# Kernel tuning notes

Hardware: AMD Instinct MI355X
Metric: run time of the kernel (lower is better)

The kernel has to match this reference:

```python
import jax, jax.numpy as jnp
import numpy as np

N_NODES = 50000
N_EDGES = 800000
F_IN = 512
HID = 256
N_CLS = 40
W_DIM = 50  # dimension*dimension*2 with dimension=5


def _prelu(x, a):
    return jnp.where(x >= 0, x, a * x)


def _segment_softmax(w, idx, n):
    # per-segment (grouped by idx), per-channel numerically stable softmax
    m = jax.ops.segment_max(w, idx, num_segments=n)
    e = jnp.exp(w - m[idx])
    s = jax.ops.segment_sum(e, idx, num_segments=n)
    return e / s[idx]


def _curvgn(x, edge_index, w_mul, W, b, w0, a, w1, b1):
    n = x.shape[0]
    h = x @ W + b                                   # [N, C]
    ow = _prelu(w_mul @ w0, a) @ w1 + b1            # [E, C] edge-weight MLP
    ow = _segment_softmax(ow, edge_index[0], n)     # softmax grouped by source (as in source)
    msg = ow * h[edge_index[0]]                     # gather x_j, weight
    return jax.ops.segment_sum(msg, edge_index[1], num_segments=n)  # scatter-add at target


def setup_inputs() -> dict:
    key = jax.random.key(0)
    ks = jax.random.split(key, 12)
    s = 0.05
    return {
        "x": jax.random.normal(ks[0], (N_NODES, F_IN), jnp.float32),
        "edge_index": jax.random.randint(ks[1], (2, N_EDGES), 0, N_NODES, jnp.int64 if jax.config.jax_enable_x64 else jnp.int32).astype(jnp.int32),
        "w_mul": jax.random.normal(ks[2], (N_EDGES, W_DIM), jnp.float32),
        "W1": jax.random.normal(ks[3], (F_IN, HID), jnp.float32) * s,
        "b1": jnp.zeros((HID,), jnp.float32),
        "m1_w0": jax.random.normal(ks[4], (W_DIM, HID), jnp.float32) * s,
        "m1_a": jnp.full((HID,), 0.2, jnp.float32),
        "m1_w1": jax.random.normal(ks[5], (HID, HID), jnp.float32) * s,
        "m1_b1": jnp.zeros((HID,), jnp.float32),
        "W2": jax.random.normal(ks[6], (HID, N_CLS), jnp.float32) * s,
        "b2": jnp.zeros((N_CLS,), jnp.float32),
        "m2_w0": jax.random.normal(ks[7], (W_DIM, N_CLS), jnp.float32) * s,
        "m2_a": jnp.full((N_CLS,), 0.2, jnp.float32),
        "m2_w1": jax.random.normal(ks[8], (N_CLS, N_CLS), jnp.float32) * s,
        "m2_b1": jnp.zeros((N_CLS,), jnp.float32),
    }


def reference(x, edge_index, w_mul, W1, b1, m1_w0, m1_a, m1_w1, m1_b1,
              W2, b2, m2_w0, m2_a, m2_w1, m2_b1):
    # eval mode: dropout is identity
    h = _curvgn(x, edge_index, w_mul, W1, b1, m1_w0, m1_a, m1_w1, m1_b1)
    h = jax.nn.elu(h)
    out = _curvgn(h, edge_index, w_mul, W2, b2, m2_w0, m2_a, m2_w1, m2_b1)
    return jax.nn.log_softmax(out, axis=1)
```

## Files before the change

### kernel.cpp

```cpp
#include <hip/hip_runtime.h>
#include <hip/hip_bf16.h>
#include <math.h>

#define N_NODESC 50000
#define N_EDGESC 800000
#define F_INC 512
#define HIDC 256
#define N_CLSC 40
#define W_DIMC 50
#define HN (2*N_NODESC)
#define NB_SCAN 196

typedef __bf16 bf16;
typedef __bf16 bf16x8 __attribute__((ext_vector_type(8)));
typedef __bf16 bf16x4 __attribute__((ext_vector_type(4)));
typedef float  f32x4  __attribute__((ext_vector_type(4)));

__global__ void k_hist(const int* __restrict__ ei, int* __restrict__ hist) {
    int e = blockIdx.x*256 + threadIdx.x;
    if (e < N_EDGESC) {
        atomicAdd(&hist[ei[e]], 1);
        atomicAdd(&hist[N_NODESC + ei[N_EDGESC + e]], 1);
    }
}
__global__ void k_copy(int* d, const int* s, int n) {
    int i = blockIdx.x*256 + threadIdx.x;
    if (i < n) d[i] = s[i];
}
__global__ void k_scan_part(const int* __restrict__ hist, int* __restrict__ part) {
    __shared__ int lds[512];
    int t = threadIdx.x;
    int i = blockIdx.x*512 + t;
    lds[t] = (i < HN) ? hist[i] : 0;
    __syncthreads();
    for (int off = 256; off > 0; off >>= 1) {
        if (t < off) lds[t] += lds[t+off];
        __syncthreads();
    }
    if (t == 0) part[blockIdx.x] = lds[0];
}
__global__ void k_scan_mid(const int* __restrict__ part, int* __restrict__ partx) {
    __shared__ int lds[256];
    int t = threadIdx.x;
    int v = (t < NB_SCAN) ? part[t] : 0;
    lds[t] = v;
    __syncthreads();
    for (int off = 1; off < 256; off <<= 1) {
        int add = (t >= off) ? lds[t-off] : 0;
        __syncthreads();
        lds[t] += add;
        __syncthreads();
    }
    partx[t] = lds[t] - v;
}
__global__ void k_scan_apply(const int* __restrict__ hist, const int* __restrict__ partx,
                             int* __restrict__ basev) {
    __shared__ int lds[512];
    int t = threadIdx.x;
    int i = blockIdx.x*512 + t;
    int v = (i < HN) ? hist[i] : 0;
    lds[t] = v;
    __syncthreads();
    for (int off = 1; off < 512; off <<= 1) {
        int add = (t >= off) ? lds[t-off] : 0;
        __syncthreads();
        lds[t] += add;
        __syncthreads();
    }
    if (i < HN) basev[i] = lds[t] - v + partx[blockIdx.x];
}
__global__ void k_scatter(const int* __restrict__ ei, int* __restrict__ cursor,
                          int* __restrict__ perm_src, int* __restrict__ perm_dst,
                          int* __restrict__ pos_dst) {
    int e = blockIdx.x*256 + threadIdx.x;
    if (e >= N_EDGESC) return;
    int s = ei[e];
    int d = ei[N_EDGESC + e];
    int p = atomicAdd(&cursor[s], 1);
    perm_src[p] = e;
    int q = atomicAdd(&cursor[N_NODESC + d], 1) - N_EDGESC;
    perm_dst[q] = e;
    pos_dst[e] = q;
}

__global__ void k_tconv(const float* __restrict__ src, bf16* __restrict__ dst,
                        int Ks, int Ns, int Kp, int Np) {
    int idx = blockIdx.x*256 + threadIdx.x;
    if (idx >= Kp*Np) return;
    int n = idx / Kp, k = idx - n*Kp;
    float v = (k < Ks && n < Ns) ? src[k*Ns + n] : 0.f;
    dst[idx] = (bf16)v;
}

__global__ __launch_bounds__(256) void k_h1(const float* __restrict__ x,
                                            const bf16* __restrict__ W1t,
                                            const float* __restrict__ b1,
                                            bf16* __restrict__ h1) {
    __shared__ bf16 a_lds[64*40];
    int tid = threadIdx.x;
    int lane = tid & 63, wv = tid >> 6;
    int l15 = lane & 15, quad = lane >> 4;
    int r0 = blockIdx.x * 64;
    f32x4 acc[4][4] = {};
    for (int ks = 0; ks < 16; ++ks) {
        #pragma unroll
        for (int i = 0; i < 2; ++i) {
            int idx = tid + i*256;
            int rl = idx >> 3, c4 = idx & 7;
            int rg = r0 + rl;
            f32x4 v = {};
            if (rg < N_NODESC) v = *(const f32x4*)&x[rg*F_INC + ks*32 + c4*4];
            bf16x4 b; b[0]=(bf16)v[0]; b[1]=(bf16)v[1]; b[2]=(bf16)v[2]; b[3]=(bf16)v[3];
            *(bf16x4*)&a_lds[rl*40 + c4*4] = b;
        }
        __syncthreads();
        bf16x8 af[4], bfr[4];
        #pragma unroll
        for (int mt = 0; mt < 4; ++mt)
            af[mt] = *(const bf16x8*)&a_lds[(mt*16 + l15)*40 + quad*8];
        #pragma unroll
        for (int nt = 0; nt < 4; ++nt) {
            int n = wv*64 + nt*16 + l15;
            bfr[nt] = *(const bf16x8*)&W1t[n*F_INC + ks*32 + quad*8];
        }
        #pragma unroll
        for (int mt = 0; mt < 4; ++mt)
            #pragma unroll
            for (int nt = 0; nt < 4; ++nt)
                acc[mt][nt] = __builtin_amdgcn_mfma_f32_16x16x32_bf16(af[mt], bfr[nt], acc[mt][nt], 0, 0, 0);
        __syncthreads();
    }
    #pragma unroll
    for (int nt = 0; nt < 4; ++nt) {
        int col = wv*64 + nt*16 + l15;
        float bias = b1[col];
        #pragma unroll
        for (int mt = 0; mt < 4; ++mt)
            #pragma unroll
            for (int r = 0; r < 4; ++r) {
                int row = r0 + mt*16 + quad*4 + r;
                if (row < N_NODESC) h1[row*HIDC + col] = (bf16)(acc[mt][nt][r] + bias);
            }
    }
}

__device__ __forceinline__ void edge_mlp1(
    int tid, const bf16* __restrict__ w0t, const float* __restrict__ a1,
    const bf16* __restrict__ w1t, const float* __restrict__ bb1,
    const bf16* wm, bf16* t1)
{
    int lane = tid & 63, wv = tid >> 6;
    int l15 = lane & 15, quad = lane >> 4;
    {
        f32x4 acc[4][4] = {};
        #pragma unroll
        for (int ks = 0; ks < 2; ++ks) {
            bf16x8 af[4], bfr[4];
            #pragma unroll
            for (int mt = 0; mt < 4; ++mt)
                af[mt] = *(const bf16x8*)&wm[(mt*16 + l15)*72 + ks*32 + quad*8];
            #pragma unroll
            for (int i = 0; i < 4; ++i) {
                int n = wv*64 + i*16 + l15;
                bfr[i] = *(const bf16x8*)&w0t[n*64 + ks*32 + quad*8];
            }
            #pragma unroll
            for (int mt = 0; mt < 4; ++mt)
                #pragma unroll
                for (int i = 0; i < 4; ++i)
                    acc[mt][i] = __builtin_amdgcn_mfma_f32_16x16x32_bf16(af[mt], bfr[i], acc[mt][i], 0, 0, 0);
        }
        #pragma unroll
        for (int i = 0; i < 4; ++i) {
            int col = wv*64 + i*16 + l15;
            float al = a1[col];
            #pragma unroll
            for (int mt = 0; mt < 4; ++mt)
                #pragma unroll
                for (int r = 0; r < 4; ++r) {
                    float v = acc[mt][i][r];
                    v = (v >= 0.f) ? v : al*v;
                    t1[(mt*16 + quad*4 + r)*264 + col] = (bf16)v;
                }
        }
    }
    __syncthreads();
    {
        f32x4 acc[4][4] = {};
        #pragma unroll
        for (int ks = 0; ks < 8; ++ks) {
            bf16x8 af[4], bfr[4];
            #pragma unroll
            for (int mt = 0; mt < 4; ++mt)
                af[mt] = *(const bf16x8*)&t1[(mt*16 + l15)*264 + ks*32 + quad*8];
            #pragma unroll
            for (int i = 0; i < 4; ++i) {
                int n = wv*64 + i*16 + l15;
                bfr[i] = *(const bf16x8*)&w1t[n*HIDC + ks*32 + quad*8];
            }
            #pragma unroll
            for (int mt = 0; mt < 4; ++mt)
                #pragma unroll
                for (int i = 0; i < 4; ++i)
                    acc[mt][i] = __builtin_amdgcn_mfma_f32_16x16x32_bf16(af[mt], bfr[i], acc[mt][i], 0, 0, 0);
        }
        __syncthreads();
        #pragma unroll
        for (int i = 0; i < 4; ++i) {
            int col = wv*64 + i*16 + l15;
            float bias = bb1[col];
            #pragma unroll
            for (int mt = 0; mt < 4; ++mt)
                #pragma unroll
                for (int r = 0; r < 4; ++r)
                    t1[(mt*16 + quad*4 + r)*264 + col] = (bf16)__expf(acc[mt][i][r] + bias);
        }
    }
    __syncthreads();
}

__device__ __forceinline__ void edge_mlp2(
    int tid, const bf16* __restrict__ w20t, const float* __restrict__ a2,
    const bf16* __restrict__ w21t, const float* __restrict__ bb2,
    const bf16* wm, bf16* t2)
{
    int lane = tid & 63, wv = tid >> 6;
    int l15 = lane & 15, quad = lane >> 4;
    {
        f32x4 acc[3] = {};
        #pragma unroll
        for (int ks = 0; ks < 2; ++ks) {
            bf16x8 af = *(const bf16x8*)&wm[(wv*16 + l15)*72 + ks*32 + quad*8];
            #pragma unroll
            for (int i = 0; i < 3; ++i) {
                bf16x8 bfr = *(const bf16x8*)&w20t[(i*16 + l15)*64 + ks*32 + quad*8];
                acc[i] = __builtin_amdgcn_mfma_f32_16x16x32_bf16(af, bfr, acc[i], 0, 0, 0);
            }
        }
        #pragma unroll
        for (int i = 0; i < 3; ++i) {
            int col = i*16 + l15;
            float al = (col < N_CLSC) ? a2[col] : 0.f;
            #pragma unroll
            for (int r = 0; r < 4; ++r) {
                float v = acc[i][r];
                v = (v >= 0.f) ? v : al*v;
                t2[(wv*16 + quad*4 + r)*72 + col] = (bf16)v;
            }
        }
    }
    __syncthreads();
    {
        f32x4 acc[3] = {};
        #pragma unroll
        for (int ks = 0; ks < 2; ++ks) {
            bf16x8 af = *(const bf16x8*)&t2[(wv*16 + l15)*72 + ks*32 + quad*8];
            #pragma unroll
            for (int i = 0; i < 3; ++i) {
                bf16x8 bfr = *(const bf16x8*)&w21t[(i*16 + l15)*64 + ks*32 + quad*8];
                acc[i] = __builtin_amdgcn_mfma_f32_16x16x32_bf16(af, bfr, acc[i], 0, 0, 0);
            }
        }
        __syncthreads();
        #pragma unroll
        for (int i = 0; i < 3; ++i) {
            int col = i*16 + l15;
            if (col < N_CLSC) {
                float bias = bb2[col];
                #pragma unroll
                for (int r = 0; r < 4; ++r)
                    t2[(wv*16 + quad*4 + r)*72 + col] = (bf16)__expf(acc[i][r] + bias);
            }
        }
    }
    __syncthreads();
}

__global__ __launch_bounds__(256) void k_passA(
    const float* __restrict__ w_mul, const int* __restrict__ perm_src,
    const int* __restrict__ ei, const int* __restrict__ pos_dst,
    const bf16* __restrict__ w0t,  const float* __restrict__ a1,
    const bf16* __restrict__ w1t,  const float* __restrict__ bb1,
    const bf16* __restrict__ w20t, const float* __restrict__ a2,
    const bf16* __restrict__ w21t, const float* __restrict__ bb2,
    float* __restrict__ s1, float* __restrict__ s2,
    bf16* __restrict__ eow1buf, bf16* __restrict__ eow2buf) {
    __shared__ bf16 wm[64*72];
    __shared__ bf16 t1[64*264];
    __shared__ bf16 t2[64*72];
    __shared__ int  e_lds[64], sv[64], pd[64];
    int tid = threadIdx.x;
    int p0 = blockIdx.x * 64;

    if (tid < 64) {
        int e = perm_src[p0 + tid];
        e_lds[tid] = e;
        sv[tid] = ei[e];
        pd[tid] = pos_dst[e];
    }
    __syncthreads();
    #pragma unroll
    for (int i = 0; i < 16; ++i) {
        int idx = tid + i*256;
        int r = idx >> 6, k = idx & 63;
        float v = (k < W_DIMC) ? w_mul[(size_t)e_lds[r]*W_DIMC + k] : 0.f;
        wm[r*72 + k] = (bf16)v;
    }
    #pragma unroll
    for (int i = 0; i < 4; ++i) {
        int idx = tid + i*256;
        int r = idx >> 4, c = 48 + (idx & 15);
        t2[r*72 + c] = (bf16)0.f;
    }
    __syncthreads();

    edge_mlp1(tid, w0t, a1, w1t, bb1, wm, t1);

    if (eow1buf) {
        int c = tid;
        for (int r = 0; r < 64; ++r)
            eow1buf[(size_t)pd[r]*HIDC + c] = t1[r*264 + c];
    }
    {
        int c = tid, r = 0;
        while (r < 64) {
            int v = sv[r];
            float acc = 0.f;
            do { acc += (float)t1[r*264 + c]; ++r; } while (r < 64 && sv[r] == v);
            atomicAdd(&s1[(size_t)v*HIDC + c], acc);
        }
    }
    __syncthreads();

    edge_mlp2(tid, w20t, a2, w21t, bb2, wm, t2);

    if (eow2buf && tid < N_CLSC) {
        int c = tid;
        for (int r = 0; r < 64; ++r)
            eow2buf[(size_t)pd[r]*N_CLSC + c] = t2[r*72 + c];
    }
    if (tid < N_CLSC) {
        int c = tid, r = 0;
        while (r < 64) {
            int v = sv[r];
            float acc = 0.f;
            do { acc += (float)t2[r*72 + c]; ++r; } while (r < 64 && sv[r] == v);
            atomicAdd(&s2[(size_t)v*N_CLSC + c], acc);
        }
    }
}

__global__ __launch_bounds__(256) void k_passB1(
    const float* __restrict__ w_mul, const int* __restrict__ perm_dst,
    const int* __restrict__ ei,
    const bf16* __restrict__ w0t, const float* __restrict__ a1,
    const bf16* __restrict__ w1t, const float* __restrict__ bb1,
    const bf16* __restrict__ g1, float* __restrict__ out1) {
    __shared__ bf16 wm[64*72];
    __shared__ bf16 t1[64*264];
    __shared__ int  e_lds[64], sv[64], dv[64];
    int tid = threadIdx.x;
    int q0 = blockIdx.x * 64;

    if (tid < 64) {
        int e = perm_dst[q0 + tid];
        e_lds[tid] = e;
        sv[tid] = ei[e];
        dv[tid] = ei[N_EDGESC + e];
    }
    __syncthreads();
    #pragma unroll
    for (int i = 0; i < 16; ++i) {
        int idx = tid + i*256;
        int r = idx >> 6, k = idx & 63;
        float v = (k < W_DIMC) ? w_mul[(size_t)e_lds[r]*W_DIMC + k] : 0.f;
        wm[r*72 + k] = (bf16)v;
    }
    __syncthreads();

    edge_mlp1(tid, w0t, a1, w1t, bb1, wm, t1);

    int c = tid, r = 0;
    while (r < 64) {
        int d = dv[r];
        float acc = 0.f;
        do {
            acc += (float)t1[r*264 + c] * (float)g1[(size_t)sv[r]*HIDC + c];
            ++r;
        } while (r < 64 && dv[r] == d);
        atomicAdd(&out1[(size_t)d*HIDC + c], acc);
    }
}
__global__ __launch_bounds__(256) void k_passB1c(
    const int* __restrict__ perm_dst, const int* __restrict__ ei,
    const bf16* __restrict__ eow1buf,
    const bf16* __restrict__ g1, float* __restrict__ out1) {
    __shared__ int sv[64], dv[64];
    int tid = threadIdx.x;
    int q0 = blockIdx.x * 64;
    if (tid < 64) {
        int e = perm_dst[q0 + tid];
        sv[tid] = ei[e];
        dv[tid] = ei[N_EDGESC + e];
    }
    __syncthreads();
    int c = tid, r = 0;
    while (r < 64) {
        int d = dv[r];
        float acc = 0.f;
        do {
            acc += (float)eow1buf[(size_t)(q0 + r)*HIDC + c] * (float)g1[(size_t)sv[r]*HIDC + c];
            ++r;
        } while (r < 64 && dv[r] == d);
        atomicAdd(&out1[(size_t)d*HIDC + c], acc);
    }
}

__global__ __launch_bounds__(256) void k_passB2(
    const float* __restrict__ w_mul, const int* __restrict__ perm_dst,
    const int* __restrict__ ei,
    const bf16* __restrict__ w20t, const float* __restrict__ a2,
    const bf16* __restrict__ w21t, const float* __restrict__ bb2,
    const bf16* __restrict__ g2, float* __restrict__ out2) {
    __shared__ bf16 wm[64*72];
    __shared__ bf16 t2[64*72];
    __shared__ int  e_lds[64], sv[64], dv[64];
    int tid = threadIdx.x;
    int q0 = blockIdx.x * 64;

    if (tid < 64) {
        int e = perm_dst[q0 + tid];
        e_lds[tid] = e;
        sv[tid] = ei[e];
        dv[tid] = ei[N_EDGESC + e];
    }
    __syncthreads();
    #pragma unroll
    for (int i = 0; i < 16; ++i) {
        int idx = tid + i*256;
        int r = idx >> 6, k = idx & 63;
        float v = (k < W_DIMC) ? w_mul[(size_t)e_lds[r]*W_DIMC + k] : 0.f;
        wm[r*72 + k] = (bf16)v;
    }
    #pragma unroll
    for (int i = 0; i < 4; ++i) {
        int idx = tid + i*256;
        int r = idx >> 4, c = 48 + (idx & 15);
        t2[r*72 + c] = (bf16)0.f;
    }
    __syncthreads();

    edge_mlp2(tid, w20t, a2, w21t, bb2, wm, t2);

    if (tid < N_CLSC) {
        int c = tid, r = 0;
        while (r < 64) {
            int d = dv[r];
            float acc = 0.f;
            do {
                acc += (float)t2[r*72 + c] * (float)g2[(size_t)sv[r]*N_CLSC + c];
                ++r;
            } while (r < 64 && dv[r] == d);
            atomicAdd(&out2[(size_t)d*N_CLSC + c], acc);
        }
    }
}
__global__ void k_passB2c(
    const int* __restrict__ perm_dst, const int* __restrict__ ei,
    const bf16* __restrict__ eow2buf,
    const bf16* __restrict__ g2, float* __restrict__ out2) {
    __shared__ int sv[64], dv[64];
    int tid = threadIdx.x;
    int q0 = blockIdx.x * 64;
    {
        int e = perm_dst[q0 + tid];
        sv[tid] = ei[e];
        dv[tid] = ei[N_EDGESC + e];
    }
    __syncthreads();
    if (tid >= N_CLSC) return;
    int c = tid, r = 0;
    while (r < 64) {
        int d = dv[r];
        float acc = 0.f;
        do {
            acc += (float)eow2buf[(size_t)(q0 + r)*N_CLSC + c] * (float)g2[(size_t)sv[r]*N_CLSC + c];
            ++r;
        } while (r < 64 && dv[r] == d);
        atomicAdd(&out2[(size_t)d*N_CLSC + c], acc);
    }
}

__global__ void k_div_bf(bf16* __restrict__ h, const float* __restrict__ s, int n) {
    int i = blockIdx.x*256 + threadIdx.x;
    if (i < n) h[i] = (bf16)((float)h[i] / s[i]);
}
__global__ void k_elu(float* __restrict__ p, int n) {
    int i = blockIdx.x*256 + threadIdx.x;
    if (i < n) { float x = p[i]; p[i] = (x > 0.f) ? x : expm1f(x); }
}
__global__ void k_h2(const float* __restrict__ out1, const float* __restrict__ W2,
                     const float* __restrict__ b2, bf16* __restrict__ h2) {
    int i = blockIdx.x*256 + threadIdx.x;
    if (i >= N_NODESC*N_CLSC) return;
    int v = i / N_CLSC, c = i - v*N_CLSC;
    float acc = b2[c];
    const float* row = &out1[(size_t)v*HIDC];
    #pragma unroll 4
    for (int k = 0; k < HIDC; ++k) acc += row[k] * W2[k*N_CLSC + c];
    h2[i] = (bf16)acc;
}
__global__ void k_lsm(const float* __restrict__ out2, float* __restrict__ out) {
    int v = blockIdx.x, c = threadIdx.x;
    bool act = (c < N_CLSC);
    float val = act ? out2[(size_t)v*N_CLSC + c] : -INFINITY;
    float m = val;
    #pragma unroll
    for (int off = 32; off > 0; off >>= 1) m = fmaxf(m, __shfl_xor(m, off));
    float ex = act ? __expf(val - m) : 0.f;
    #pragma unroll
    for (int off = 32; off > 0; off >>= 1) ex += __shfl_xor(ex, off);
    if (act) out[(size_t)v*N_CLSC + c] = val - m - logf(ex);
}

extern "C" void kernel_launch(void* const* d_in, const int* in_sizes, int n_in,
                              void* d_out, int out_size, void* d_ws, size_t ws_size,
                              hipStream_t stream) {
    const float* x    = (const float*)d_in[0];
    const int*   ei   = (const int*)d_in[1];
    const float* wmul = (const float*)d_in[2];
    const float* W1   = (const float*)d_in[3];
    const float* b1   = (const float*)d_in[4];
    const float* m1w0 = (const float*)d_in[5];
    const float* m1a  = (const float*)d_in[6];
    const float* m1w1 = (const float*)d_in[7];
    const float* m1b1 = (const float*)d_in[8];
    const float* W2   = (const float*)d_in[9];
    const float* b2   = (const float*)d_in[10];
    const float* m2w0 = (const float*)d_in[11];
    const float* m2a  = (const float*)d_in[12];
    const float* m2w1 = (const float*)d_in[13];
    const float* m2b1 = (const float*)d_in[14];
    float* out = (float*)d_out;

    char* ws = (char*)d_ws;
    size_t off = 0;
    auto alloc = [&](size_t bytes) -> void* {
        off = (off + 255) & ~(size_t)255;
        void* p = ws + off;
        off += bytes;
        return p;
    };
    bf16*  h1g1  = (bf16*) alloc((size_t)N_NODESC*HIDC*2);
    float* s1o1  = (float*)alloc((size_t)N_NODESC*HIDC*4);
    bf16*  h2g2  = (bf16*) alloc((size_t)N_NODESC*N_CLSC*2);
    float* s2o2  = (float*)alloc((size_t)N_NODESC*N_CLSC*4);
    bf16*  W1t   = (bf16*) alloc(256*512*2);
    bf16*  w0t   = (bf16*) alloc(256*64*2);
    bf16*  w1tm  = (bf16*) alloc(256*256*2);
    bf16*  w20t  = (bf16*) alloc(48*64*2);
    bf16*  w21t  = (bf16*) alloc(48*64*2);
    int*   hist  = (int*)  alloc(HN*4);
    int*   basev = (int*)  alloc(HN*4);
    int*   cursor= (int*)  alloc(HN*4);
    int*   part  = (int*)  alloc(256*4);
    int*   partx = (int*)  alloc(256*4);
    int*   perm_src = (int*)alloc((size_t)N_EDGESC*4);
    int*   perm_dst = (int*)alloc((size_t)N_EDGESC*4);
    int*   pos_dst  = (int*)alloc((size_t)N_EDGESC*4);
    size_t need_cache = (size_t)N_EDGESC*HIDC*2 + (size_t)N_EDGESC*N_CLSC*2 + 512;
    bool use_cache = (off + need_cache) <= ws_size;
    bf16* eow1buf = nullptr;
    bf16* eow2buf = nullptr;
    if (use_cache) {
        eow1buf = (bf16*)alloc((size_t)N_EDGESC*HIDC*2);
        eow2buf = (bf16*)alloc((size_t)N_EDGESC*N_CLSC*2);
    }

    hipMemsetAsync(hist, 0, HN*4, stream);
    hipMemsetAsync(s1o1, 0, (size_t)N_NODESC*HIDC*4, stream);
    hipMemsetAsync(s2o2, 0, (size_t)N_NODESC*N_CLSC*4, stream);
    k_hist<<<(N_EDGESC+255)/256, 256, 0, stream>>>(ei, hist);
    k_scan_part<<<NB_SCAN, 512, 0, stream>>>(hist, part);
    k_scan_mid<<<1, 256, 0, stream>>>(part, partx);
    k_scan_apply<<<NB_SCAN, 512, 0, stream>>>(hist, partx, basev);
    k_copy<<<(HN+255)/256, 256, 0, stream>>>(cursor, basev, HN);
    k_scatter<<<(N_EDGESC+255)/256, 256, 0, stream>>>(ei, cursor, perm_src, perm_dst, pos_dst);

    k_tconv<<<(512*256+255)/256, 256, 0, stream>>>(W1,   W1t, 512, 256, 512, 256);
    k_tconv<<<(256*64+255)/256,  256, 0, stream>>>(m1w0, w0t,  50, 256,  64, 256);
    k_tconv<<<(256*256+255)/256, 256, 0, stream>>>(m1w1, w1tm, 256, 256, 256, 256);
    k_tconv<<<(48*64+255)/256,   256, 0, stream>>>(m2w0, w20t,  50,  40,  64,  48);
    k_tconv<<<(48*64+255)/256,   256, 0, stream>>>(m2w1, w21t,  40,  40,  64,  48);

    k_h1<<<(N_NODESC+63)/64, 256, 0, stream>>>(x, W1t, b1, h1g1);
    k_passA<<<N_EDGESC/64, 256, 0, stream>>>(wmul, perm_src, ei, pos_dst,
                                             w0t, m1a, w1tm, m1b1,
                                             w20t, m2a, w21t, m2b1,
                                             s1o1, s2o2, eow1buf, eow2buf);
    k_div_bf<<<(N_NODESC*HIDC+255)/256, 256, 0, stream>>>(h1g1, s1o1, N_NODESC*HIDC);
    hipMemsetAsync(s1o1, 0, (size_t)N_NODESC*HIDC*4, stream);
    if (use_cache)
        k_passB1c<<<N_EDGESC/64, 256, 0, stream>>>(perm_dst, ei, eow1buf, h1g1, s1o1);
    else
        k_passB1<<<N_EDGESC/64, 256, 0, stream>>>(wmul, perm_dst, ei,
                                                  w0t, m1a, w1tm, m1b1, h1g1, s1o1);
    k_elu<<<(N_NODESC*HIDC+255)/256, 256, 0, stream>>>(s1o1, N_NODESC*HIDC);

    k_h2<<<(N_NODESC*N_CLSC+255)/256, 256, 0, stream>>>(s1o1, W2, b2, h2g2);
    k_div_bf<<<(N_NODESC*N_CLSC+255)/256, 256, 0, stream>>>(h2g2, s2o2, N_NODESC*N_CLSC);
    hipMemsetAsync(s2o2, 0, (size_t)N_NODESC*N_CLSC*4, stream);
    if (use_cache)
        k_passB2c<<<N_EDGESC/64, 64, 0, stream>>>(perm_dst, ei, eow2buf, h2g2, s2o2);
    else
        k_passB2<<<N_EDGESC/64, 256, 0, stream>>>(wmul, perm_dst, ei,
                                                  w20t, m2a, w21t, m2b1, h2g2, s2o2);
    k_lsm<<<N_NODESC, 64, 0, stream>>>(s2o2, out);
}
```

Measured before the change: 1.816 ms.

## Store edge weights in source order and aggregate per destination via CSR gather

The edge-MLP kernel now writes the exponentiated edge weights contiguously in source-sorted order instead of scattering them to destination positions. The scatter step records, for each destination-sorted slot, the source-sorted position and the source node. New per-node gather kernels (one block per destination node) then sum weight times feature with no atomics, and they also absorb the ELU and log-softmax epilogues. This removes the output memsets, the atomic scatter-add, the separate elementwise kernels and the non-cached fallback path, and it vectorises the divide kernel. In exchange the gathers read the weight rows indirectly, per-node blocks are unbalanced by degree, and the weight cache is now allocated unconditionally, which assumes the workspace is large enough.

```diff
diff --git a/kernel.cpp b/kernel.cpp
--- a/kernel.cpp
+++ b/kernel.cpp
@@ -70,8 +70,8 @@
     if (i < HN) basev[i] = lds[t] - v + partx[blockIdx.x];
 }
 __global__ void k_scatter(const int* __restrict__ ei, int* __restrict__ cursor,
-                          int* __restrict__ perm_src, int* __restrict__ perm_dst,
-                          int* __restrict__ pos_dst) {
+                          int* __restrict__ perm_src,
+                          int* __restrict__ spd, int* __restrict__ svd) {
     int e = blockIdx.x*256 + threadIdx.x;
     if (e >= N_EDGESC) return;
     int s = ei[e];
@@ -79,8 +79,8 @@
     int p = atomicAdd(&cursor[s], 1);
     perm_src[p] = e;
     int q = atomicAdd(&cursor[N_NODESC + d], 1) - N_EDGESC;
-    perm_dst[q] = e;
-    pos_dst[e] = q;
+    spd[q] = p;
+    svd[q] = s;
 }
 
 __global__ void k_tconv(const float* __restrict__ src, bf16* __restrict__ dst,
@@ -96,7 +96,7 @@
                                             const bf16* __restrict__ W1t,
                                             const float* __restrict__ b1,
                                             bf16* __restrict__ h1) {
-    __shared__ bf16 a_lds[64*40];
+    __shared__ __align__(16) bf16 a_lds[64*40];
     int tid = threadIdx.x;
     int lane = tid & 63, wv = tid >> 6;
     int l15 = lane & 15, quad = lane >> 4;
@@ -109,7 +109,7 @@
             int rl = idx >> 3, c4 = idx & 7;
             int rg = r0 + rl;
             f32x4 v = {};
-            if (rg < N_NODESC) v = *(const f32x4*)&x[rg*F_INC + ks*32 + c4*4];
+            if (rg < N_NODESC) v = *(const f32x4*)&x[(size_t)rg*F_INC + ks*32 + c4*4];
             bf16x4 b; b[0]=(bf16)v[0]; b[1]=(bf16)v[1]; b[2]=(bf16)v[2]; b[3]=(bf16)v[3];
             *(bf16x4*)&a_lds[rl*40 + c4*4] = b;
         }
@@ -139,18 +139,50 @@
             #pragma unroll
             for (int r = 0; r < 4; ++r) {
                 int row = r0 + mt*16 + quad*4 + r;
-                if (row < N_NODESC) h1[row*HIDC + col] = (bf16)(acc[mt][nt][r] + bias);
-            }
-    }
-}
-
-__device__ __forceinline__ void edge_mlp1(
-    int tid, const bf16* __restrict__ w0t, const float* __restrict__ a1,
-    const bf16* __restrict__ w1t, const float* __restrict__ bb1,
-    const bf16* wm, bf16* t1)
-{
+                if (row < N_NODESC) h1[(size_t)row*HIDC + col] = (bf16)(acc[mt][nt][r] + bias);
+            }
+    }
+}
+
+__global__ __launch_bounds__(256) void k_edge(
+    const float* __restrict__ w_mul, const int* __restrict__ perm_src,
+    const int* __restrict__ ei,
+    const bf16* __restrict__ w0t,  const float* __restrict__ a1,
+    const bf16* __restrict__ w1t,  const float* __restrict__ bb1,
+    const bf16* __restrict__ w20t, const float* __restrict__ a2,
+    const bf16* __restrict__ w21t, const float* __restrict__ bb2,
+    float* __restrict__ s1, float* __restrict__ s2,
+    bf16* __restrict__ eow1, bf16* __restrict__ eow2) {
+    __shared__ __align__(16) bf16 wm[64*72];
+    __shared__ __align__(16) bf16 t1[64*264];
+    __shared__ __align__(16) bf16 t2[64*72];
+    __shared__ int e_lds[64], sv[64];
+    int tid = threadIdx.x;
     int lane = tid & 63, wv = tid >> 6;
     int l15 = lane & 15, quad = lane >> 4;
+    int p0 = blockIdx.x * 64;
+
+    if (tid < 64) {
+        int e = perm_src[p0 + tid];
+        e_lds[tid] = e;
+        sv[tid] = ei[e];
+    }
+    __syncthreads();
+    #pragma unroll
+    for (int i = 0; i < 16; ++i) {
+        int idx = tid + i*256;
+        int r = idx >> 6, k = idx & 63;
+        float v = (k < W_DIMC) ? w_mul[(size_t)e_lds[r]*W_DIMC + k] : 0.f;
+        wm[r*72 + k] = (bf16)v;
+    }
+    #pragma unroll
+    for (int i = 0; i < 4; ++i) {
+        int idx = tid + i*256;
+        int r = idx >> 4, c = 48 + (idx & 15);
+        t2[r*72 + c] = (bf16)0.f;
+    }
+    __syncthreads();
+
     {
         f32x4 acc[4][4] = {};
         #pragma unroll
@@ -185,6 +217,7 @@
         }
     }
     __syncthreads();
+
     {
         f32x4 acc[4][4] = {};
         #pragma unroll
@@ -217,15 +250,27 @@
         }
     }
     __syncthreads();
-}
-
-__device__ __forceinline__ void edge_mlp2(
-    int tid, const bf16* __restrict__ w20t, const float* __restrict__ a2,
-    const bf16* __restrict__ w21t, const float* __restrict__ bb2,
-    const bf16* wm, bf16* t2)
-{
-    int lane = tid & 63, wv = tid >> 6;
-    int l15 = lane & 15, quad = lane >> 4;
+
+    #pragma unroll
+    for (int i = 0; i < 8; ++i) {
+        int idx = i*256 + tid;
+        int row = idx >> 5, c8 = idx & 31;
+        bf16x8 v = *(const bf16x8*)&t1[row*264 + c8*8];
+        *(bf16x8*)&eow1[(size_t)(p0 + row)*HIDC + c8*8] = v;
+    }
+    {
+        int c = tid;
+        float acc = 0.f;
+        #pragma unroll 8
+        for (int r = 0; r < 64; ++r) {
+            acc += (float)t1[r*264 + c];
+            if (r == 63 || sv[r+1] != sv[r]) {
+                atomicAdd(&s1[(size_t)sv[r]*HIDC + c], acc);
+                acc = 0.f;
+            }
+        }
+    }
+
     {
         f32x4 acc[3] = {};
         #pragma unroll
@@ -250,6 +295,7 @@
         }
     }
     __syncthreads();
+
     {
         f32x4 acc[3] = {};
         #pragma unroll
@@ -274,230 +320,78 @@
         }
     }
     __syncthreads();
-}
-
-__global__ __launch_bounds__(256) void k_passA(
-    const float* __restrict__ w_mul, const int* __restrict__ perm_src,
-    const int* __restrict__ ei, const int* __restrict__ pos_dst,
-    const bf16* __restrict__ w0t,  const float* __restrict__ a1,
-    const bf16* __restrict__ w1t,  const float* __restrict__ bb1,
-    const bf16* __restrict__ w20t, const float* __restrict__ a2,
-    const bf16* __restrict__ w21t, const float* __restrict__ bb2,
-    float* __restrict__ s1, float* __restrict__ s2,
-    bf16* __restrict__ eow1buf, bf16* __restrict__ eow2buf) {
-    __shared__ bf16 wm[64*72];
-    __shared__ bf16 t1[64*264];
-    __shared__ bf16 t2[64*72];
-    __shared__ int  e_lds[64], sv[64], pd[64];
-    int tid = threadIdx.x;
-    int p0 = blockIdx.x * 64;
-
-    if (tid < 64) {
-        int e = perm_src[p0 + tid];
-        e_lds[tid] = e;
-        sv[tid] = ei[e];
-        pd[tid] = pos_dst[e];
-    }
-    __syncthreads();
-    #pragma unroll
-    for (int i = 0; i < 16; ++i) {
-        int idx = tid + i*256;
-        int r = idx >> 6, k = idx & 63;
-        float v = (k < W_DIMC) ? w_mul[(size_t)e_lds[r]*W_DIMC + k] : 0.f;
-        wm[r*72 + k] = (bf16)v;
-    }
-    #pragma unroll
-    for (int i = 0; i < 4; ++i) {
-        int idx = tid + i*256;
-        int r = idx >> 4, c = 48 + (idx & 15);
-        t2[r*72 + c] = (bf16)0.f;
-    }
-    __syncthreads();
-
-    edge_mlp1(tid, w0t, a1, w1t, bb1, wm, t1);
-
-    if (eow1buf) {
-        int c = tid;
-        for (int r = 0; r < 64; ++r)
-            eow1buf[(size_t)pd[r]*HIDC + c] = t1[r*264 + c];
-    }
-    {
-        int c = tid, r = 0;
-        while (r < 64) {
-            int v = sv[r];
-            float acc = 0.f;
-            do { acc += (float)t1[r*264 + c]; ++r; } while (r < 64 && sv[r] == v);
-            atomicAdd(&s1[(size_t)v*HIDC + c], acc);
-        }
-    }
-    __syncthreads();
-
-    edge_mlp2(tid, w20t, a2, w21t, bb2, wm, t2);
-
-    if (eow2buf && tid < N_CLSC) {
-        int c = tid;
-        for (int r = 0; r < 64; ++r)
-            eow2buf[(size_t)pd[r]*N_CLSC + c] = t2[r*72 + c];
-    }
-    if (tid < N_CLSC) {
-        int c = tid, r = 0;
-        while (r < 64) {
-            int v = sv[r];
-            float acc = 0.f;
-            do { acc += (float)t2[r*72 + c]; ++r; } while (r < 64 && sv[r] == v);
-            atomicAdd(&s2[(size_t)v*N_CLSC + c], acc);
-        }
-    }
-}
-
-__global__ __launch_bounds__(256) void k_passB1(
-    const float* __restrict__ w_mul, const int* __restrict__ perm_dst,
-    const int* __restrict__ ei,
-    const bf16* __restrict__ w0t, const float* __restrict__ a1,
-    const bf16* __restrict__ w1t, const float* __restrict__ bb1,
-    const bf16* __restrict__ g1, float* __restrict__ out1) {
-    __shared__ bf16 wm[64*72];
-    __shared__ bf16 t1[64*264];
-    __shared__ int  e_lds[64], sv[64], dv[64];
-    int tid = threadIdx.x;
-    int q0 = blockIdx.x * 64;
-
-    if (tid < 64) {
-        int e = perm_dst[q0 + tid];
-        e_lds[tid] = e;
-        sv[tid] = ei[e];
-        dv[tid] = ei[N_EDGESC + e];
-    }
-    __syncthreads();
-    #pragma unroll
-    for (int i = 0; i < 16; ++i) {
-        int idx = tid + i*256;
-        int r = idx >> 6, k = idx & 63;
-        float v = (k < W_DIMC) ? w_mul[(size_t)e_lds[r]*W_DIMC + k] : 0.f;
-        wm[r*72 + k] = (bf16)v;
-    }
-    __syncthreads();
-
-    edge_mlp1(tid, w0t, a1, w1t, bb1, wm, t1);
-
-    int c = tid, r = 0;
-    while (r < 64) {
-        int d = dv[r];
+
+    #pragma unroll
+    for (int i = 0; i < 2; ++i) {
+        int idx = i*256 + tid;
+        if (idx < 320) {
+            int row = idx / 5, c8 = idx % 5;
+            bf16x8 v = *(const bf16x8*)&t2[row*72 + c8*8];
+            *(bf16x8*)&eow2[(size_t)(p0 + row)*N_CLSC + c8*8] = v;
+        }
+    }
+    if (tid < 240) {
+        int c = tid % 40, g = tid / 40;
+        int rA = g*11, rB = (rA + 11 < 64) ? rA + 11 : 64;
         float acc = 0.f;
-        do {
-            acc += (float)t1[r*264 + c] * (float)g1[(size_t)sv[r]*HIDC + c];
-            ++r;
-        } while (r < 64 && dv[r] == d);
-        atomicAdd(&out1[(size_t)d*HIDC + c], acc);
-    }
-}
-__global__ __launch_bounds__(256) void k_passB1c(
-    const int* __restrict__ perm_dst, const int* __restrict__ ei,
-    const bf16* __restrict__ eow1buf,
-    const bf16* __restrict__ g1, float* __restrict__ out1) {
-    __shared__ int sv[64], dv[64];
-    int tid = threadIdx.x;
-    int q0 = blockIdx.x * 64;
-    if (tid < 64) {
-        int e = perm_dst[q0 + tid];
-        sv[tid] = ei[e];
-        dv[tid] = ei[N_EDGESC + e];
-    }
-    __syncthreads();
-    int c = tid, r = 0;
-    while (r < 64) {
-        int d = dv[r];
-        float acc = 0.f;
-        do {
-            acc += (float)eow1buf[(size_t)(q0 + r)*HIDC + c] * (float)g1[(size_t)sv[r]*HIDC + c];
-            ++r;
-        } while (r < 64 && dv[r] == d);
-        atomicAdd(&out1[(size_t)d*HIDC + c], acc);
-    }
-}
-
-__global__ __launch_bounds__(256) void k_passB2(
-    const float* __restrict__ w_mul, const int* __restrict__ perm_dst,
-    const int* __restrict__ ei,
-    const bf16* __restrict__ w20t, const float* __restrict__ a2,
-    const bf16* __restrict__ w21t, const float* __restrict__ bb2,
-    const bf16* __restrict__ g2, float* __restrict__ out2) {
-    __shared__ bf16 wm[64*72];
-    __shared__ bf16 t2[64*72];
-    __shared__ int  e_lds[64], sv[64], dv[64];
-    int tid = threadIdx.x;
-    int q0 = blockIdx.x * 64;
-
-    if (tid < 64) {
-        int e = perm_dst[q0 + tid];
-        e_lds[tid] = e;
-        sv[tid] = ei[e];
-        dv[tid] = ei[N_EDGESC + e];
-    }
-    __syncthreads();
-    #pragma unroll
-    for (int i = 0; i < 16; ++i) {
-        int idx = tid + i*256;
-        int r = idx >> 6, k = idx & 63;
-        float v = (k < W_DIMC) ? w_mul[(size_t)e_lds[r]*W_DIMC + k] : 0.f;
-        wm[r*72 + k] = (bf16)v;
-    }
-    #pragma unroll
-    for (int i = 0; i < 4; ++i) {
-        int idx = tid + i*256;
-        int r = idx >> 4, c = 48 + (idx & 15);
-        t2[r*72 + c] = (bf16)0.f;
-    }
-    __syncthreads();
-
-    edge_mlp2(tid, w20t, a2, w21t, bb2, wm, t2);
-
-    if (tid < N_CLSC) {
-        int c = tid, r = 0;
-        while (r < 64) {
-            int d = dv[r];
-            float acc = 0.f;
-            do {
-                acc += (float)t2[r*72 + c] * (float)g2[(size_t)sv[r]*N_CLSC + c];
-                ++r;
-            } while (r < 64 && dv[r] == d);
-            atomicAdd(&out2[(size_t)d*N_CLSC + c], acc);
-        }
-    }
-}
-__global__ void k_passB2c(
-    const int* __restrict__ perm_dst, const int* __restrict__ ei,
-    const bf16* __restrict__ eow2buf,
-    const bf16* __restrict__ g2, float* __restrict__ out2) {
-    __shared__ int sv[64], dv[64];
-    int tid = threadIdx.x;
-    int q0 = blockIdx.x * 64;
-    {
-        int e = perm_dst[q0 + tid];
-        sv[tid] = ei[e];
-        dv[tid] = ei[N_EDGESC + e];
-    }
-    __syncthreads();
-    if (tid >= N_CLSC) return;
-    int c = tid, r = 0;
-    while (r < 64) {
-        int d = dv[r];
-        float acc = 0.f;
-        do {
-            acc += (float)eow2buf[(size_t)(q0 + r)*N_CLSC + c] * (float)g2[(size_t)sv[r]*N_CLSC + c];
-            ++r;
-        } while (r < 64 && dv[r] == d);
-        atomicAdd(&out2[(size_t)d*N_CLSC + c], acc);
-    }
-}
-
-__global__ void k_div_bf(bf16* __restrict__ h, const float* __restrict__ s, int n) {
+        for (int r = rA; r < rB; ++r) {
+            acc += (float)t2[r*72 + c];
+            if (r == rB-1 || sv[r+1] != sv[r]) {
+                atomicAdd(&s2[(size_t)sv[r]*N_CLSC + c], acc);
+                acc = 0.f;
+            }
+        }
+    }
+}
+
+__global__ __launch_bounds__(256) void k_agg1(
+    const bf16* __restrict__ eow1, const bf16* __restrict__ g1,
+    const int* __restrict__ basev, const int* __restrict__ spd,
+    const int* __restrict__ svd, float* __restrict__ out1) {
+    int v = blockIdx.x, c = threadIdx.x;
+    int b = basev[N_NODESC + v] - N_EDGESC;
+    int e = (v < N_NODESC-1) ? basev[N_NODESC + v + 1] - N_EDGESC : N_EDGESC;
+    float acc = 0.f;
+    #pragma unroll 2
+    for (int j = b; j < e; ++j) {
+        int sp = spd[j], s = svd[j];
+        acc += (float)eow1[(size_t)sp*HIDC + c] * (float)g1[(size_t)s*HIDC + c];
+    }
+    out1[(size_t)v*HIDC + c] = (acc > 0.f) ? acc : expm1f(acc);
+}
+
+__global__ __launch_bounds__(64) void k_agg2(
+    const bf16* __restrict__ eow2, const bf16* __restrict__ g2,
+    const int* __restrict__ basev, const int* __restrict__ spd,
+    const int* __restrict__ svd, float* __restrict__ out) {
+    int v = blockIdx.x, c = threadIdx.x;
+    int b = basev[N_NODESC + v] - N_EDGESC;
+    int e = (v < N_NODESC-1) ? basev[N_NODESC + v + 1] - N_EDGESC : N_EDGESC;
+    bool act = (c < N_CLSC);
+    float acc = 0.f;
+    #pragma unroll 2
+    for (int j = b; j < e; ++j) {
+        int sp = spd[j], s = svd[j];
+        if (act) acc += (float)eow2[(size_t)sp*N_CLSC + c] * (float)g2[(size_t)s*N_CLSC + c];
+    }
+    float m = act ? acc : -INFINITY;
+    #pragma unroll
+    for (int off = 32; off > 0; off >>= 1) m = fmaxf(m, __shfl_xor(m, off));
+    float ex = act ? __expf(acc - m) : 0.f;
+    #pragma unroll
+    for (int off = 32; off > 0; off >>= 1) ex += __shfl_xor(ex, off);
+    if (act) out[(size_t)v*N_CLSC + c] = acc - m - logf(ex);
+}
+
+__global__ void k_div_bf4(bf16* __restrict__ h, const float* __restrict__ s, int n4) {
     int i = blockIdx.x*256 + threadIdx.x;
-    if (i < n) h[i] = (bf16)((float)h[i] / s[i]);
-}
-__global__ void k_elu(float* __restrict__ p, int n) {
-    int i = blockIdx.x*256 + threadIdx.x;
-    if (i < n) { float x = p[i]; p[i] = (x > 0.f) ? x : expm1f(x); }
+    if (i < n4) {
+        bf16x4 hv = *(bf16x4*)&h[i*4];
+        f32x4 sv = *(const f32x4*)&s[i*4];
+        #pragma unroll
+        for (int k = 0; k < 4; ++k) hv[k] = (bf16)((float)hv[k] / sv[k]);
+        *(bf16x4*)&h[i*4] = hv;
+    }
 }
 __global__ void k_h2(const float* __restrict__ out1, const float* __restrict__ W2,
                      const float* __restrict__ b2, bf16* __restrict__ h2) {
@@ -509,18 +403,6 @@
     #pragma unroll 4
     for (int k = 0; k < HIDC; ++k) acc += row[k] * W2[k*N_CLSC + c];
     h2[i] = (bf16)acc;
-}
-__global__ void k_lsm(const float* __restrict__ out2, float* __restrict__ out) {
-    int v = blockIdx.x, c = threadIdx.x;
-    bool act = (c < N_CLSC);
-    float val = act ? out2[(size_t)v*N_CLSC + c] : -INFINITY;
-    float m = val;
-    #pragma unroll
-    for (int off = 32; off > 0; off >>= 1) m = fmaxf(m, __shfl_xor(m, off));
-    float ex = act ? __expf(val - m) : 0.f;
-    #pragma unroll
-    for (int off = 32; off > 0; off >>= 1) ex += __shfl_xor(ex, off);
-    if (act) out[(size_t)v*N_CLSC + c] = val - m - logf(ex);
 }
 
 extern "C" void kernel_launch(void* const* d_in, const int* in_sizes, int n_in,
@@ -554,7 +436,7 @@
     bf16*  h1g1  = (bf16*) alloc((size_t)N_NODESC*HIDC*2);
     float* s1o1  = (float*)alloc((size_t)N_NODESC*HIDC*4);
     bf16*  h2g2  = (bf16*) alloc((size_t)N_NODESC*N_CLSC*2);
-    float* s2o2  = (float*)alloc((size_t)N_NODESC*N_CLSC*4);
+    float* s2    = (float*)alloc((size_t)N_NODESC*N_CLSC*4);
     bf16*  W1t   = (bf16*) alloc(256*512*2);
     bf16*  w0t   = (bf16*) alloc(256*64*2);
     bf16*  w1tm  = (bf16*) alloc(256*256*2);
@@ -566,26 +448,20 @@
     int*   part  = (int*)  alloc(256*4);
     int*   partx = (int*)  alloc(256*4);
     int*   perm_src = (int*)alloc((size_t)N_EDGESC*4);
-    int*   perm_dst = (int*)alloc((size_t)N_EDGESC*4);
-    int*   pos_dst  = (int*)alloc((size_t)N_EDGESC*4);
-    size_t need_cache = (size_t)N_EDGESC*HIDC*2 + (size_t)N_EDGESC*N_CLSC*2 + 512;
-    bool use_cache = (off + need_cache) <= ws_size;
-    bf16* eow1buf = nullptr;
-    bf16* eow2buf = nullptr;
-    if (use_cache) {
-        eow1buf = (bf16*)alloc((size_t)N_EDGESC*HIDC*2);
-        eow2buf = (bf16*)alloc((size_t)N_EDGESC*N_CLSC*2);
-    }
+    int*   spd      = (int*)alloc((size_t)N_EDGESC*4);
+    int*   svd      = (int*)alloc((size_t)N_EDGESC*4);
+    bf16*  eow1  = (bf16*) alloc((size_t)N_EDGESC*HIDC*2);
+    bf16*  eow2  = (bf16*) alloc((size_t)N_EDGESC*N_CLSC*2);
 
     hipMemsetAsync(hist, 0, HN*4, stream);
     hipMemsetAsync(s1o1, 0, (size_t)N_NODESC*HIDC*4, stream);
-    hipMemsetAsync(s2o2, 0, (size_t)N_NODESC*N_CLSC*4, stream);
+    hipMemsetAsync(s2,   0, (size_t)N_NODESC*N_CLSC*4, stream);
     k_hist<<<(N_EDGESC+255)/256, 256, 0, stream>>>(ei, hist);
     k_scan_part<<<NB_SCAN, 512, 0, stream>>>(hist, part);
     k_scan_mid<<<1, 256, 0, stream>>>(part, partx);
     k_scan_apply<<<NB_SCAN, 512, 0, stream>>>(hist, partx, basev);
     k_copy<<<(HN+255)/256, 256, 0, stream>>>(cursor, basev, HN);
-    k_scatter<<<(N_EDGESC+255)/256, 256, 0, stream>>>(ei, cursor, perm_src, perm_dst, pos_dst);
+    k_scatter<<<(N_EDGESC+255)/256, 256, 0, stream>>>(ei, cursor, perm_src, spd, svd);
 
     k_tconv<<<(512*256+255)/256, 256, 0, stream>>>(W1,   W1t, 512, 256, 512, 256);
     k_tconv<<<(256*64+255)/256,  256, 0, stream>>>(m1w0, w0t,  50, 256,  64, 256);
@@ -594,26 +470,14 @@
     k_tconv<<<(48*64+255)/256,   256, 0, stream>>>(m2w1, w21t,  40,  40,  64,  48);
 
     k_h1<<<(N_NODESC+63)/64, 256, 0, stream>>>(x, W1t, b1, h1g1);
-    k_passA<<<N_EDGESC/64, 256, 0, stream>>>(wmul, perm_src, ei, pos_dst,
-                                             w0t, m1a, w1tm, m1b1,
-                                             w20t, m2a, w21t, m2b1,
-                                             s1o1, s2o2, eow1buf, eow2buf);
-    k_div_bf<<<(N_NODESC*HIDC+255)/256, 256, 0, stream>>>(h1g1, s1o1, N_NODESC*HIDC);
-    hipMemsetAsync(s1o1, 0, (size_t)N_NODESC*HIDC*4, stream);
-    if (use_cache)
-        k_passB1c<<<N_EDGESC/64, 256, 0, stream>>>(perm_dst, ei, eow1buf, h1g1, s1o1);
-    else
-        k_passB1<<<N_EDGESC/64, 256, 0, stream>>>(wmul, perm_dst, ei,
-                                                  w0t, m1a, w1tm, m1b1, h1g1, s1o1);
-    k_elu<<<(N_NODESC*HIDC+255)/256, 256, 0, stream>>>(s1o1, N_NODESC*HIDC);
+    k_edge<<<N_EDGESC/64, 256, 0, stream>>>(wmul, perm_src, ei,
+                                            w0t, m1a, w1tm, m1b1,
+                                            w20t, m2a, w21t, m2b1,
+                                            s1o1, s2, eow1, eow2);
+    k_div_bf4<<<(N_NODESC*HIDC/4+255)/256, 256, 0, stream>>>(h1g1, s1o1, N_NODESC*HIDC/4);
+    k_agg1<<<N_NODESC, 256, 0, stream>>>(eow1, h1g1, basev, spd, svd, s1o1);
 
     k_h2<<<(N_NODESC*N_CLSC+255)/256, 256, 0, stream>>>(s1o1, W2, b2, h2g2);
-    k_div_bf<<<(N_NODESC*N_CLSC+255)/256, 256, 0, stream>>>(h2g2, s2o2, N_NODESC*N_CLSC);
-    hipMemsetAsync(s2o2, 0, (size_t)N_NODESC*N_CLSC*4, stream);
-    if (use_cache)
-        k_passB2c<<<N_EDGESC/64, 64, 0, stream>>>(perm_dst, ei, eow2buf, h2g2, s2o2);
-    else
-        k_passB2<<<N_EDGESC/64, 256, 0, stream>>>(wmul, perm_dst, ei,
-                                                  w20t, m2a, w21t, m2b1, h2g2, s2o2);
-    k_lsm<<<N_NODESC, 64, 0, stream>>>(s2o2, out);
-}
+    k_div_bf4<<<(N_NODESC*N_CLSC/4+255)/256, 256, 0, stream>>>(h2g2, s2, N_NODESC*N_CLSC/4);
+    k_agg2<<<N_NODESC, 64, 0, stream>>>(eow2, h2g2, basev, spd, svd, out);
+}
```

New measurement: 1.583 ms. -12.8%, faster.
